# Kernel optimization log

Measured on AMD Instinct MI355X. Metric: run time of the kernel, lower is better.

## Reference

```python
import jax, jax.numpy as jnp
import numpy as np

DIM, H, DH = 3072, 24, 128
MLP = int(DIM * 4.0)
EPS = 1e-6


def setup_inputs() -> dict:
    key = jax.random.key(0)
    ks = jax.random.split(key, 8)
    B, L = 2, 4096
    s = 0.02
    return {
        "hidden_states": jax.random.normal(ks[0], (B, L, DIM), jnp.float32),
        "temb": jax.random.normal(ks[1], (B, DIM), jnp.float32),
        "rope": jax.random.normal(ks[2], (L, DH // 2, 4), jnp.float32),
        "w_lin": jax.random.normal(ks[3], (DIM, 3 * DIM), jnp.float32) * s,
        "b_lin": jnp.zeros((3 * DIM,), jnp.float32),
        "w1": jax.random.normal(ks[4], (DIM, 3 * DIM + MLP), jnp.float32) * s,
        "b1": jnp.zeros((3 * DIM + MLP,), jnp.float32),
        "w2": jax.random.normal(ks[5], (DIM + MLP, DIM), jnp.float32) * s,
        "b2": jnp.zeros((DIM,), jnp.float32),
        "q_scale": jnp.ones((DH,), jnp.float32),
        "k_scale": jnp.ones((DH,), jnp.float32),
    }


def _rms(x, scale):
    return x * jax.lax.rsqrt(jnp.mean(x * x, axis=-1, keepdims=True) + EPS) * scale


def _rope(x, fr):
    # x: [B,H,L,DH]; fr: [L, DH//2, 2, 2]
    B, Hn, L, D = x.shape
    x_ = x.reshape(B, Hn, L, D // 2, 1, 2)
    out = fr[..., 0] * x_[..., 0] + fr[..., 1] * x_[..., 1]  # [B,H,L,D//2,2]
    return out.reshape(B, Hn, L, D)


def reference(hidden_states, temb, rope, w_lin, b_lin, w1, b1, w2, b2, q_scale, k_scale):
    B, L, _ = hidden_states.shape
    residual = hidden_states
    # AdaLayerNormZeroSingle
    emb = jax.nn.silu(temb) @ w_lin + b_lin  # [B, 3*DIM]
    shift, scale, gate = jnp.split(emb[:, None, :], 3, axis=-1)
    mu = jnp.mean(hidden_states, axis=-1, keepdims=True)
    var = jnp.mean(jnp.square(hidden_states - mu), axis=-1, keepdims=True)
    x = (hidden_states - mu) * jax.lax.rsqrt(var + EPS)
    x = x * (1 + scale) + shift
    # fused QKV + MLP projection
    proj = x @ w1 + b1
    qkv, mlp = proj[..., : 3 * DIM], proj[..., 3 * DIM :]
    qkv = qkv.reshape(B, L, 3, H, DH).transpose(2, 0, 3, 1, 4)  # [3,B,H,L,DH]
    q, k, v = qkv[0], qkv[1], qkv[2]
    q = _rms(q, q_scale)
    k = _rms(k, k_scale)
    fr = rope.reshape(L, DH // 2, 2, 2)
    q = _rope(q, fr)
    k = _rope(k, fr)
    # heads are MERGED before attention (faithful to source)
    q = q.transpose(0, 2, 1, 3).reshape(B, L, H * DH)
    k = k.transpose(0, 2, 1, 3).reshape(B, L, H * DH)
    v = v.transpose(0, 2, 1, 3).reshape(B, L, H * DH)
    attn = jax.nn.softmax(jnp.einsum("bqd,bkd->bqk", q, k) * (DH ** -0.5), axis=-1)
    attn_out = jnp.einsum("bqk,bkd->bqd", attn, v)
    h = jnp.concatenate([attn_out, jax.nn.gelu(mlp)], axis=-1) @ w2 + b2
    return residual + gate * h
```

## Files before the change

### kernel.cpp

```cpp
#include <hip/hip_runtime.h>
#include <hip/hip_fp16.h>

typedef _Float16 half_t;
typedef __attribute__((ext_vector_type(8))) _Float16 f16x8;
typedef __attribute__((ext_vector_type(4))) float f32x4;

#define DIM   3072
#define NH    24
#define DH    128
#define MLP_D 12288
#define LSEQ  4096
#define BATCH 2
#define NROWS 8192
#define N1    21504
#define QKV_N 9216
#define CAT_N 15360

__device__ __forceinline__ void gload16(const void* g, void* l) {
  __builtin_amdgcn_global_load_lds((const __attribute__((address_space(1))) void*)g,
                                   (__attribute__((address_space(3))) void*)l, 16, 0, 0);
}

__device__ __forceinline__ float gelu_tanh(float x) {
  float u = 0.7978845608028654f * (x + 0.044715f * x * x * x);
  float t = 1.f - 2.f / (__expf(2.f * u) + 1.f);
  return 0.5f * x * (1.f + t);
}

struct EpiParams {
  const float* bias;
  float* outF; int ldoF;
  half_t* o1; int ldo1;
  half_t* o2; int ldo2;
  const float* resid;
  const float* gate;
  float scale;
};

template<int EPI>
__global__ __launch_bounds__(512, 2) void gemm256(
    const half_t* __restrict__ A, int lda,
    const half_t* __restrict__ B, int ldb,
    int nbx, int nby, int nsplit, int K, EpiParams ep)
{
  __shared__ __align__(16) char lds[131072];
  const int t = threadIdx.x, lane = t & 63, wid = t >> 6;

  const int nwg = nbx * nby;
  const int wg = blockIdx.x;
  const int id = (wg & 7) * (nwg >> 3) + (wg >> 3);
  const int panel = 8 * nbx;
  const int bm = (id / panel) * 8 + (id % 8);
  const int bn = (id % panel) / 8;
  const int brow = bm * 256, bcol = bn * 256;
  const int wr = wid >> 2, wc = wid & 3;

  f32x4 acc[8][4];
#pragma unroll
  for (int m = 0; m < 8; ++m)
#pragma unroll
    for (int n = 0; n < 4; ++n) acc[m][n] = (f32x4){0.f, 0.f, 0.f, 0.f};

  const int scol = (((lane & 3) ^ ((lane >> 3) & 3)) * 8);
  const half_t* pA = A + (size_t)(brow + wid * 32 + (lane >> 2)) * lda + scol;
  const half_t* pB = B + (size_t)(bcol + wid * 32 + (lane >> 2)) * ldb + scol;
  const int wrow = wid * 2048;
  const int NT = K >> 6;

  const int pc = (((lane >> 4) ^ ((lane >> 1) & 3)) << 4);
  const int aoff = (wr * 128 + (lane & 15)) * 64 + pc;
  const int boff = 32768 + (wc * 64 + (lane & 15)) * 64 + pc;

  f16x8 af[2][4], bf[2][4];

#define STAGE_A(bb, kh, tk) {                                               \
    gload16(pA + (size_t)(tk) * 64 + (kh) * 32,                             \
            (bb) + (kh) * 16384 + wrow);                                    \
    gload16(pA + (size_t)(tk) * 64 + (kh) * 32 + (size_t)16 * lda,          \
            (bb) + (kh) * 16384 + wrow + 1024); }
#define STAGE_B(bb, kh, tk) {                                               \
    gload16(pB + (size_t)(tk) * 64 + (kh) * 32,                             \
            (bb) + 32768 + (kh) * 16384 + wrow);                            \
    gload16(pB + (size_t)(tk) * 64 + (kh) * 32 + (size_t)16 * ldb,          \
            (bb) + 32768 + (kh) * 16384 + wrow + 1024); }

#define MFMA_Q(accoff, ab, bb2)                                             \
    _Pragma("unroll")                                                       \
    for (int mi = 0; mi < 4; ++mi)                                          \
      _Pragma("unroll")                                                     \
      for (int nj = 0; nj < 4; ++nj)                                        \
        acc[(accoff) + mi][nj] = __builtin_amdgcn_mfma_f32_16x16x32_f16(    \
            af[ab][mi], bf[bb2][nj], acc[(accoff) + mi][nj], 0, 0, 0);

  {
    char* b0 = lds;
    char* b1 = lds + 65536;
    STAGE_B(b0, 0, 0); STAGE_A(b0, 0, 0); STAGE_B(b0, 1, 0); STAGE_A(b0, 1, 0);
    STAGE_B(b1, 0, 1); STAGE_A(b1, 0, 1); STAGE_B(b1, 1, 1); STAGE_A(b1, 1, 1);
    asm volatile("s_waitcnt vmcnt(8)" ::: "memory");
    __builtin_amdgcn_s_barrier();
#pragma unroll
    for (int mi = 0; mi < 4; ++mi) af[0][mi] = *(const f16x8*)(lds + aoff + mi * 1024);
#pragma unroll
    for (int nj = 0; nj < 4; ++nj) bf[0][nj] = *(const f16x8*)(lds + boff + nj * 1024);
    __builtin_amdgcn_s_barrier();
  }

  for (int tt = 0; tt < NT; ++tt) {
    char* cb = lds + (size_t)(tt & 1) * 65536;
    char* nb = lds + (size_t)((tt & 1) ^ 1) * 65536;

    __builtin_amdgcn_s_setprio(1);
    MFMA_Q(0, 0, 0)
    __builtin_amdgcn_s_setprio(0);
#pragma unroll
    for (int mi = 0; mi < 4; ++mi) af[1][mi] = *(const f16x8*)(cb + aoff + 4096 + mi * 1024);
    if (tt + 2 < NT) STAGE_B(cb, 0, tt + 2);
    __builtin_amdgcn_s_barrier();

    __builtin_amdgcn_s_setprio(1);
    MFMA_Q(4, 1, 0)
    __builtin_amdgcn_s_setprio(0);
#pragma unroll
    for (int mi = 0; mi < 4; ++mi) af[0][mi] = *(const f16x8*)(cb + aoff + 16384 + mi * 1024);
#pragma unroll
    for (int nj = 0; nj < 4; ++nj) bf[1][nj] = *(const f16x8*)(cb + boff + 16384 + nj * 1024);
    if (tt + 2 < NT) STAGE_A(cb, 0, tt + 2);
    __builtin_amdgcn_s_barrier();

    __builtin_amdgcn_s_setprio(1);
    MFMA_Q(0, 0, 1)
    __builtin_amdgcn_s_setprio(0);
#pragma unroll
    for (int mi = 0; mi < 4; ++mi) af[1][mi] = *(const f16x8*)(cb + aoff + 16384 + 4096 + mi * 1024);
    if (tt + 2 < NT) STAGE_B(cb, 1, tt + 2);
    if (tt + 2 < NT) asm volatile("s_waitcnt vmcnt(6)" ::: "memory");
    else             asm volatile("s_waitcnt vmcnt(0)" ::: "memory");
    __builtin_amdgcn_s_barrier();

    __builtin_amdgcn_s_setprio(1);
    MFMA_Q(4, 1, 1)
    __builtin_amdgcn_s_setprio(0);
    if (tt + 1 < NT) {
#pragma unroll
      for (int mi = 0; mi < 4; ++mi) af[0][mi] = *(const f16x8*)(nb + aoff + mi * 1024);
#pragma unroll
      for (int nj = 0; nj < 4; ++nj) bf[0][nj] = *(const f16x8*)(nb + boff + nj * 1024);
    }
    if (tt + 2 < NT) STAGE_A(cb, 1, tt + 2);
    __builtin_amdgcn_s_barrier();
  }
#undef STAGE_A
#undef STAGE_B
#undef MFMA_Q

  const int laneR = lane & 15;
  const int colb = bcol + wc * 64;
  const int rowb = brow + wr * 128 + (lane >> 4) * 4;
#pragma unroll
  for (int mi = 0; mi < 8; ++mi) {
#pragma unroll
    for (int nj = 0; nj < 4; ++nj) {
      int col = colb + nj * 16 + laneR;
#pragma unroll
      for (int j = 0; j < 4; ++j) {
        int row = rowb + mi * 16 + j;
        float v = acc[mi][nj][j];
        if (EPI == 0) {
          v += ep.bias[col];
          if (col < nsplit) {
            ep.o1[(size_t)row * ep.ldo1 + col] = (half_t)v;
          } else {
            ep.o2[(size_t)row * ep.ldo2 + DIM + (col - nsplit)] = (half_t)gelu_tanh(v);
          }
        } else if (EPI == 1) {
          ep.o1[(size_t)row * ep.ldo1 + col] = (half_t)(v * ep.scale);
        } else if (EPI == 2) {
          ep.o2[(size_t)row * ep.ldo2 + col] = (half_t)v;
        } else {
          v += ep.bias[col];
          int b = row >> 12;
          float g = ep.gate[(size_t)b * QKV_N + col];
          float r = ep.resid[(size_t)row * DIM + col];
          ep.outF[(size_t)row * ep.ldoF + col] = r + g * v;
        }
      }
    }
  }
}

__global__ __launch_bounds__(256) void k_emb(
    const float* __restrict__ temb, const float* __restrict__ w_lin,
    const float* __restrict__ b_lin, float* __restrict__ emb)
{
  __shared__ float s[DIM];
  int b = blockIdx.y;
  int col = blockIdx.x * 256 + threadIdx.x;
  const float* tr = temb + (size_t)b * DIM;
  for (int k = threadIdx.x; k < DIM; k += 256) {
    float x = tr[k];
    s[k] = x / (1.f + __expf(-x));
  }
  __syncthreads();
  float acc = b_lin[col];
  for (int k = 0; k < DIM; k += 4) {
    acc += s[k] * w_lin[(size_t)k * QKV_N + col]
         + s[k + 1] * w_lin[(size_t)(k + 1) * QKV_N + col]
         + s[k + 2] * w_lin[(size_t)(k + 2) * QKV_N + col]
         + s[k + 3] * w_lin[(size_t)(k + 3) * QKV_N + col];
  }
  emb[(size_t)b * QKV_N + col] = acc;
}

__global__ __launch_bounds__(256) void k_lnmod(
    const float* __restrict__ hs, const float* __restrict__ emb,
    half_t* __restrict__ xmod)
{
  int row = blockIdx.x;
  int b = row >> 12;
  const float* x = hs + (size_t)row * DIM;
  int t = threadIdx.x;
  float s = 0.f, s2 = 0.f;
  float4 v[3];
#pragma unroll
  for (int i = 0; i < 3; ++i) {
    v[i] = ((const float4*)x)[t + 256 * i];
    s  += v[i].x + v[i].y + v[i].z + v[i].w;
    s2 += v[i].x * v[i].x + v[i].y * v[i].y + v[i].z * v[i].z + v[i].w * v[i].w;
  }
  for (int o = 32; o; o >>= 1) { s += __shfl_xor(s, o); s2 += __shfl_xor(s2, o); }
  __shared__ float rs[4], rs2[4];
  int lane = t & 63, w = t >> 6;
  if (lane == 0) { rs[w] = s; rs2[w] = s2; }
  __syncthreads();
  s = rs[0] + rs[1] + rs[2] + rs[3];
  s2 = rs2[0] + rs2[1] + rs2[2] + rs2[3];
  float mu = s * (1.f / DIM);
  float var = s2 * (1.f / DIM) - mu * mu;
  float rstd = rsqrtf(var + 1e-6f);
  const float* shift = emb + (size_t)b * QKV_N;
  const float* scale = shift + DIM;
#pragma unroll
  for (int i = 0; i < 3; ++i) {
    int g = t + 256 * i;
    float4 sc = ((const float4*)scale)[g];
    float4 sh = ((const float4*)shift)[g];
    half_t ob[4];
    float vv[4] = {v[i].x, v[i].y, v[i].z, v[i].w};
    float scv[4] = {sc.x, sc.y, sc.z, sc.w};
    float shv[4] = {sh.x, sh.y, sh.z, sh.w};
#pragma unroll
    for (int j = 0; j < 4; ++j) {
      float xn = (vv[j] - mu) * rstd;
      ob[j] = (half_t)(xn * (1.f + scv[j]) + shv[j]);
    }
    *(uint2*)&xmod[(size_t)row * DIM + g * 4] = *(uint2*)ob;
  }
}

__global__ __launch_bounds__(256) void k_transpose_cvt(
    const float* __restrict__ in, half_t* __restrict__ out, int R, int C)
{
  __shared__ float s[64][65];
  int c0 = blockIdx.x * 64, r0 = blockIdx.y * 64;
  int tx = threadIdx.x & 63, ty = threadIdx.x >> 6;
#pragma unroll
  for (int j = 0; j < 16; ++j) {
    int r = ty + j * 4;
    s[r][tx] = in[(size_t)(r0 + r) * C + c0 + tx];
  }
  __syncthreads();
#pragma unroll
  for (int j = 0; j < 16; ++j) {
    int c = ty + j * 4;
    out[(size_t)(c0 + c) * R + r0 + tx] = (half_t)s[tx][c];
  }
}

__global__ __launch_bounds__(256) void k_qk_rmsrope(
    half_t* __restrict__ qkv, const float* __restrict__ rope,
    const float* __restrict__ q_scale, const float* __restrict__ k_scale)
{
  int w = blockIdx.x * 4 + (threadIdx.x >> 6);
  int lane = threadIdx.x & 63;
  int qk = w & 1;
  int hr = w >> 1;
  int h = hr % 24;
  int bl = hr / 24;
  size_t base = (size_t)bl * QKV_N + qk * DIM + h * DH;
  float x0 = (float)qkv[base + lane * 2];
  float x1 = (float)qkv[base + lane * 2 + 1];
  float ss = x0 * x0 + x1 * x1;
  for (int o = 32; o; o >>= 1) ss += __shfl_xor(ss, o);
  float r = rsqrtf(ss * (1.f / DH) + 1e-6f);
  const float* sc = qk ? k_scale : q_scale;
  float xs0 = x0 * r * sc[lane * 2];
  float xs1 = x1 * r * sc[lane * 2 + 1];
  int l = bl & (LSEQ - 1);
  float4 fr = ((const float4*)rope)[(size_t)l * 64 + lane];
  qkv[base + lane * 2]     = (half_t)(fr.x * xs0 + fr.y * xs1);
  qkv[base + lane * 2 + 1] = (half_t)(fr.z * xs0 + fr.w * xs1);
}

__global__ __launch_bounds__(256) void k_vT(
    const half_t* __restrict__ qkv, half_t* __restrict__ vT)
{
  __shared__ half_t s[64][65];
  int b = blockIdx.z;
  int l0 = blockIdx.x * 64, d0 = blockIdx.y * 64;
  int tx = threadIdx.x & 63, ty = threadIdx.x >> 6;
#pragma unroll
  for (int j = 0; j < 16; ++j) {
    int l = ty + j * 4;
    s[l][tx] = qkv[(size_t)(b * LSEQ + l0 + l) * QKV_N + 2 * DIM + d0 + tx];
  }
  __syncthreads();
#pragma unroll
  for (int j = 0; j < 16; ++j) {
    int d = ty + j * 4;
    vT[((size_t)b * DIM + d0 + d) * LSEQ + l0 + tx] = s[tx][d];
  }
}

__global__ __launch_bounds__(256) void k_softmax(
    const half_t* __restrict__ S, half_t* __restrict__ P)
{
  int row = blockIdx.x;
  const half_t* srow = S + (size_t)row * LSEQ;
  int t = threadIdx.x;
  f16x8 hv[2];
  float vf[16];
  float mx = -1e30f;
#pragma unroll
  for (int i = 0; i < 2; ++i) {
    hv[i] = ((const f16x8*)srow)[t + 256 * i];
#pragma unroll
    for (int j = 0; j < 8; ++j) {
      vf[i * 8 + j] = (float)hv[i][j];
      mx = fmaxf(mx, vf[i * 8 + j]);
    }
  }
  for (int o = 32; o; o >>= 1) mx = fmaxf(mx, __shfl_xor(mx, o));
  __shared__ float rmx[4], rsum[4];
  int lane = t & 63, w = t >> 6;
  if (lane == 0) rmx[w] = mx;
  __syncthreads();
  mx = fmaxf(fmaxf(rmx[0], rmx[1]), fmaxf(rmx[2], rmx[3]));
  float s = 0.f;
#pragma unroll
  for (int i = 0; i < 16; ++i) {
    vf[i] = __expf(vf[i] - mx);
    s += vf[i];
  }
  for (int o = 32; o; o >>= 1) s += __shfl_xor(s, o);
  if (lane == 0) rsum[w] = s;
  __syncthreads();
  s = rsum[0] + rsum[1] + rsum[2] + rsum[3];
  float inv = 1.f / s;
#pragma unroll
  for (int i = 0; i < 2; ++i) {
    f16x8 ob;
#pragma unroll
    for (int j = 0; j < 8; ++j) ob[j] = (half_t)(vf[i * 8 + j] * inv);
    ((f16x8*)&P[(size_t)row * LSEQ])[t + 256 * i] = ob;
  }
}

extern "C" void kernel_launch(void* const* d_in, const int* in_sizes, int n_in,
                              void* d_out, int out_size, void* d_ws, size_t ws_size,
                              hipStream_t stream) {
  const float* hs      = (const float*)d_in[0];
  const float* temb    = (const float*)d_in[1];
  const float* rope    = (const float*)d_in[2];
  const float* w_lin   = (const float*)d_in[3];
  const float* b_lin   = (const float*)d_in[4];
  const float* w1      = (const float*)d_in[5];
  const float* b1      = (const float*)d_in[6];
  const float* w2      = (const float*)d_in[7];
  const float* b2      = (const float*)d_in[8];
  const float* q_scale = (const float*)d_in[9];
  const float* k_scale = (const float*)d_in[10];
  float* out = (float*)d_out;

  char* ws = (char*)d_ws;
  size_t off = 0;
  auto alloc = [&](size_t bytes) { char* p = ws + off; off += (bytes + 255) & ~(size_t)255; return p; };
  float*  emb    = (float*) alloc((size_t)BATCH * QKV_N * 4);
  half_t* xmod   = (half_t*)alloc((size_t)NROWS * DIM * 2);
  half_t* w1T    = (half_t*)alloc((size_t)N1 * DIM * 2);
  half_t* w2T    = (half_t*)alloc((size_t)DIM * CAT_N * 2);
  half_t* qkv    = (half_t*)alloc((size_t)NROWS * QKV_N * 2);
  half_t* concat = (half_t*)alloc((size_t)NROWS * CAT_N * 2);
  half_t* vT     = (half_t*)alloc((size_t)BATCH * DIM * LSEQ * 2);
  half_t* Sbuf   = (half_t*)alloc((size_t)LSEQ * LSEQ * 2);
  half_t* Pbuf   = (half_t*)alloc((size_t)LSEQ * LSEQ * 2);
  (void)ws_size; (void)n_in; (void)in_sizes; (void)out_size;

  k_emb<<<dim3(QKV_N / 256, BATCH), 256, 0, stream>>>(temb, w_lin, b_lin, emb);
  k_transpose_cvt<<<dim3(N1 / 64, DIM / 64), 256, 0, stream>>>(w1, w1T, DIM, N1);
  k_transpose_cvt<<<dim3(DIM / 64, CAT_N / 64), 256, 0, stream>>>(w2, w2T, CAT_N, DIM);
  k_lnmod<<<NROWS, 256, 0, stream>>>(hs, emb, xmod);

  EpiParams ep1 = {b1, nullptr, 0, qkv, QKV_N, concat, CAT_N, nullptr, nullptr, 0.f};
  gemm256<0><<<(N1 / 256) * (NROWS / 256), 512, 0, stream>>>(
      xmod, DIM, w1T, DIM, N1 / 256, NROWS / 256, QKV_N, DIM, ep1);

  k_qk_rmsrope<<<(NROWS * NH * 2) / 4, 256, 0, stream>>>(qkv, rope, q_scale, k_scale);
  k_vT<<<dim3(LSEQ / 64, DIM / 64, BATCH), 256, 0, stream>>>(qkv, vT);

  for (int b = 0; b < BATCH; ++b) {
    const half_t* qb = qkv + (size_t)b * LSEQ * QKV_N;
    EpiParams epS = {nullptr, nullptr, 0, Sbuf, LSEQ, nullptr, 0, nullptr, nullptr, 0.08838834764831845f};
    gemm256<1><<<(LSEQ / 256) * (LSEQ / 256), 512, 0, stream>>>(
        qb, QKV_N, qb + DIM, QKV_N, LSEQ / 256, LSEQ / 256, 0, DIM, epS);
    k_softmax<<<LSEQ, 256, 0, stream>>>(Sbuf, Pbuf);
    EpiParams epPV = {nullptr, nullptr, 0, nullptr, 0,
                      concat + (size_t)b * LSEQ * CAT_N, CAT_N, nullptr, nullptr, 0.f};
    gemm256<2><<<(DIM / 256) * (LSEQ / 256), 512, 0, stream>>>(
        Pbuf, LSEQ, vT + (size_t)b * DIM * LSEQ, LSEQ, DIM / 256, LSEQ / 256, 0, LSEQ, epPV);
  }

  EpiParams ep2 = {b2, out, DIM, nullptr, 0, nullptr, 0, hs, emb + 2 * DIM, 0.f};
  gemm256<3><<<(DIM / 256) * (NROWS / 256), 512, 0, stream>>>(
      concat, CAT_N, w2T, CAT_N, DIM / 256, NROWS / 256, 0, CAT_N, ep2);
}
```

Baseline: 2.788 ms.

## Batch attention GEMMs across batch and merge small prologue kernels

Result: no change. 2.779 ms (-0.3%).

```diff
diff --git a/kernel.cpp b/kernel.cpp
--- a/kernel.cpp
+++ b/kernel.cpp
@@ -41,19 +41,24 @@
 __global__ __launch_bounds__(512, 2) void gemm256(
     const half_t* __restrict__ A, int lda,
     const half_t* __restrict__ B, int ldb,
-    int nbx, int nby, int nsplit, int K, EpiParams ep)
+    int nbx, int nper, size_t strA, size_t strB, size_t strO,
+    int nsplit, int K, EpiParams ep)
 {
   __shared__ __align__(16) char lds[131072];
   const int t = threadIdx.x, lane = t & 63, wid = t >> 6;
 
-  const int nwg = nbx * nby;
+  const int nwg = gridDim.x;
   const int wg = blockIdx.x;
   const int id = (wg & 7) * (nwg >> 3) + (wg >> 3);
+  const int bz = id / nper;
+  const int rid = id - bz * nper;
   const int panel = 8 * nbx;
-  const int bm = (id / panel) * 8 + (id % 8);
-  const int bn = (id % panel) / 8;
+  const int bm = (rid / panel) * 8 + (rid % 8);
+  const int bn = (rid % panel) / 8;
   const int brow = bm * 256, bcol = bn * 256;
   const int wr = wid >> 2, wc = wid & 3;
+  A += bz * strA;
+  B += bz * strB;
 
   f32x4 acc[8][4];
 #pragma unroll
@@ -154,6 +159,10 @@
 #undef STAGE_B
 #undef MFMA_Q
 
+  half_t* o1 = ep.o1;
+  half_t* o2 = ep.o2;
+  if (EPI == 1) o1 += (size_t)bz * strO;
+  if (EPI == 2) o2 += (size_t)bz * strO;
   const int laneR = lane & 15;
   const int colb = bcol + wc * 64;
   const int rowb = brow + wr * 128 + (lane >> 4) * 4;
@@ -169,14 +178,14 @@
         if (EPI == 0) {
           v += ep.bias[col];
           if (col < nsplit) {
-            ep.o1[(size_t)row * ep.ldo1 + col] = (half_t)v;
+            o1[(size_t)row * ep.ldo1 + col] = (half_t)v;
           } else {
-            ep.o2[(size_t)row * ep.ldo2 + DIM + (col - nsplit)] = (half_t)gelu_tanh(v);
+            o2[(size_t)row * ep.ldo2 + DIM + (col - nsplit)] = (half_t)gelu_tanh(v);
           }
         } else if (EPI == 1) {
-          ep.o1[(size_t)row * ep.ldo1 + col] = (half_t)(v * ep.scale);
+          o1[(size_t)row * ep.ldo1 + col] = (half_t)(v * ep.scale);
         } else if (EPI == 2) {
-          ep.o2[(size_t)row * ep.ldo2 + col] = (half_t)v;
+          o2[(size_t)row * ep.ldo2 + col] = (half_t)v;
         } else {
           v += ep.bias[col];
           int b = row >> 12;
@@ -189,27 +198,71 @@
   }
 }
 
-__global__ __launch_bounds__(256) void k_emb(
+__device__ __forceinline__ void tp_tile(
+    const float* __restrict__ in, half_t* __restrict__ out, int R, int C,
+    int r0, int c0, float (*s)[65], int t)
+{
+  const int tx = t & 15, ty = t >> 4;
+#pragma unroll
+  for (int j = 0; j < 4; ++j) {
+    int r = ty + j * 16;
+    float4 v = *(const float4*)&in[(size_t)(r0 + r) * C + c0 + tx * 4];
+    s[r][tx * 4 + 0] = v.x; s[r][tx * 4 + 1] = v.y;
+    s[r][tx * 4 + 2] = v.z; s[r][tx * 4 + 3] = v.w;
+  }
+  __syncthreads();
+#pragma unroll
+  for (int j = 0; j < 4; ++j) {
+    int c = ty + j * 16;
+    half_t o[4] = {(half_t)s[tx * 4 + 0][c], (half_t)s[tx * 4 + 1][c],
+                   (half_t)s[tx * 4 + 2][c], (half_t)s[tx * 4 + 3][c]};
+    *(uint2*)&out[(size_t)(c0 + c) * R + r0 + tx * 4] = *(uint2*)o;
+  }
+}
+
+#define NBW1 ((N1 / 64) * (DIM / 64))
+#define NBW2 ((DIM / 64) * (CAT_N / 64))
+#define NBEMB ((QKV_N / 256) * BATCH)
+
+__global__ __launch_bounds__(256) void k_pre(
+    const float* __restrict__ w1, half_t* __restrict__ w1T,
+    const float* __restrict__ w2, half_t* __restrict__ w2T,
     const float* __restrict__ temb, const float* __restrict__ w_lin,
     const float* __restrict__ b_lin, float* __restrict__ emb)
 {
-  __shared__ float s[DIM];
-  int b = blockIdx.y;
-  int col = blockIdx.x * 256 + threadIdx.x;
-  const float* tr = temb + (size_t)b * DIM;
-  for (int k = threadIdx.x; k < DIM; k += 256) {
-    float x = tr[k];
-    s[k] = x / (1.f + __expf(-x));
-  }
-  __syncthreads();
-  float acc = b_lin[col];
-  for (int k = 0; k < DIM; k += 4) {
-    acc += s[k] * w_lin[(size_t)k * QKV_N + col]
-         + s[k + 1] * w_lin[(size_t)(k + 1) * QKV_N + col]
-         + s[k + 2] * w_lin[(size_t)(k + 2) * QKV_N + col]
-         + s[k + 3] * w_lin[(size_t)(k + 3) * QKV_N + col];
-  }
-  emb[(size_t)b * QKV_N + col] = acc;
+  __shared__ float s[64][65];
+  int id = blockIdx.x;
+  if (id < NBW1) {
+    int cx = id % (N1 / 64), ry = id / (N1 / 64);
+    tp_tile(w1, w1T, DIM, N1, ry * 64, cx * 64, s, threadIdx.x);
+    return;
+  }
+  id -= NBW1;
+  if (id < NBW2) {
+    int cx = id % (DIM / 64), ry = id / (DIM / 64);
+    tp_tile(w2, w2T, CAT_N, DIM, ry * 64, cx * 64, s, threadIdx.x);
+    return;
+  }
+  id -= NBW2;
+  {
+    float* sf = &s[0][0];
+    int b = id / (QKV_N / 256);
+    int col = (id % (QKV_N / 256)) * 256 + threadIdx.x;
+    const float* tr = temb + (size_t)b * DIM;
+    for (int k = threadIdx.x; k < DIM; k += 256) {
+      float x = tr[k];
+      sf[k] = x / (1.f + __expf(-x));
+    }
+    __syncthreads();
+    float acc = b_lin[col];
+    for (int k = 0; k < DIM; k += 4) {
+      acc += sf[k] * w_lin[(size_t)k * QKV_N + col]
+           + sf[k + 1] * w_lin[(size_t)(k + 1) * QKV_N + col]
+           + sf[k + 2] * w_lin[(size_t)(k + 2) * QKV_N + col]
+           + sf[k + 3] * w_lin[(size_t)(k + 3) * QKV_N + col];
+    }
+    emb[(size_t)b * QKV_N + col] = acc;
+  }
 }
 
 __global__ __launch_bounds__(256) void k_lnmod(
@@ -258,67 +311,56 @@
   }
 }
 
-__global__ __launch_bounds__(256) void k_transpose_cvt(
-    const float* __restrict__ in, half_t* __restrict__ out, int R, int C)
-{
-  __shared__ float s[64][65];
-  int c0 = blockIdx.x * 64, r0 = blockIdx.y * 64;
-  int tx = threadIdx.x & 63, ty = threadIdx.x >> 6;
-#pragma unroll
-  for (int j = 0; j < 16; ++j) {
-    int r = ty + j * 4;
-    s[r][tx] = in[(size_t)(r0 + r) * C + c0 + tx];
-  }
-  __syncthreads();
-#pragma unroll
-  for (int j = 0; j < 16; ++j) {
-    int c = ty + j * 4;
-    out[(size_t)(c0 + c) * R + r0 + tx] = (half_t)s[tx][c];
-  }
-}
-
-__global__ __launch_bounds__(256) void k_qk_rmsrope(
+#define NROPE ((NROWS * NH * 2) / 4)
+#define NVT   ((LSEQ / 64) * (DIM / 64) * BATCH)
+
+__global__ __launch_bounds__(256) void k_ropevt(
     half_t* __restrict__ qkv, const float* __restrict__ rope,
-    const float* __restrict__ q_scale, const float* __restrict__ k_scale)
-{
-  int w = blockIdx.x * 4 + (threadIdx.x >> 6);
-  int lane = threadIdx.x & 63;
-  int qk = w & 1;
-  int hr = w >> 1;
-  int h = hr % 24;
-  int bl = hr / 24;
-  size_t base = (size_t)bl * QKV_N + qk * DIM + h * DH;
-  float x0 = (float)qkv[base + lane * 2];
-  float x1 = (float)qkv[base + lane * 2 + 1];
-  float ss = x0 * x0 + x1 * x1;
-  for (int o = 32; o; o >>= 1) ss += __shfl_xor(ss, o);
-  float r = rsqrtf(ss * (1.f / DH) + 1e-6f);
-  const float* sc = qk ? k_scale : q_scale;
-  float xs0 = x0 * r * sc[lane * 2];
-  float xs1 = x1 * r * sc[lane * 2 + 1];
-  int l = bl & (LSEQ - 1);
-  float4 fr = ((const float4*)rope)[(size_t)l * 64 + lane];
-  qkv[base + lane * 2]     = (half_t)(fr.x * xs0 + fr.y * xs1);
-  qkv[base + lane * 2 + 1] = (half_t)(fr.z * xs0 + fr.w * xs1);
-}
-
-__global__ __launch_bounds__(256) void k_vT(
-    const half_t* __restrict__ qkv, half_t* __restrict__ vT)
+    const float* __restrict__ q_scale, const float* __restrict__ k_scale,
+    half_t* __restrict__ vT)
 {
   __shared__ half_t s[64][65];
-  int b = blockIdx.z;
-  int l0 = blockIdx.x * 64, d0 = blockIdx.y * 64;
-  int tx = threadIdx.x & 63, ty = threadIdx.x >> 6;
-#pragma unroll
-  for (int j = 0; j < 16; ++j) {
-    int l = ty + j * 4;
-    s[l][tx] = qkv[(size_t)(b * LSEQ + l0 + l) * QKV_N + 2 * DIM + d0 + tx];
-  }
-  __syncthreads();
-#pragma unroll
-  for (int j = 0; j < 16; ++j) {
-    int d = ty + j * 4;
-    vT[((size_t)b * DIM + d0 + d) * LSEQ + l0 + tx] = s[tx][d];
+  int id = blockIdx.x;
+  if (id < NROPE) {
+    int w = id * 4 + (threadIdx.x >> 6);
+    int lane = threadIdx.x & 63;
+    int qk = w & 1;
+    int hr = w >> 1;
+    int h = hr % 24;
+    int bl = hr / 24;
+    size_t base = (size_t)bl * QKV_N + qk * DIM + h * DH;
+    float x0 = (float)qkv[base + lane * 2];
+    float x1 = (float)qkv[base + lane * 2 + 1];
+    float ss = x0 * x0 + x1 * x1;
+    for (int o = 32; o; o >>= 1) ss += __shfl_xor(ss, o);
+    float r = rsqrtf(ss * (1.f / DH) + 1e-6f);
+    const float* sc = qk ? k_scale : q_scale;
+    float xs0 = x0 * r * sc[lane * 2];
+    float xs1 = x1 * r * sc[lane * 2 + 1];
+    int l = bl & (LSEQ - 1);
+    float4 fr = ((const float4*)rope)[(size_t)l * 64 + lane];
+    qkv[base + lane * 2]     = (half_t)(fr.x * xs0 + fr.y * xs1);
+    qkv[base + lane * 2 + 1] = (half_t)(fr.z * xs0 + fr.w * xs1);
+    return;
+  }
+  id -= NROPE;
+  {
+    int nb = (LSEQ / 64) * (DIM / 64);
+    int b = id / nb;
+    int rem = id % nb;
+    int l0 = (rem % (LSEQ / 64)) * 64, d0 = (rem / (LSEQ / 64)) * 64;
+    int tx = threadIdx.x & 63, ty = threadIdx.x >> 6;
+#pragma unroll
+    for (int j = 0; j < 16; ++j) {
+      int l = ty + j * 4;
+      s[l][tx] = qkv[(size_t)(b * LSEQ + l0 + l) * QKV_N + 2 * DIM + d0 + tx];
+    }
+    __syncthreads();
+#pragma unroll
+    for (int j = 0; j < 16; ++j) {
+      int d = ty + j * 4;
+      vT[((size_t)b * DIM + d0 + d) * LSEQ + l0 + tx] = s[tx][d];
+    }
   }
 }
 
@@ -392,35 +434,34 @@
   half_t* qkv    = (half_t*)alloc((size_t)NROWS * QKV_N * 2);
   half_t* concat = (half_t*)alloc((size_t)NROWS * CAT_N * 2);
   half_t* vT     = (half_t*)alloc((size_t)BATCH * DIM * LSEQ * 2);
-  half_t* Sbuf   = (half_t*)alloc((size_t)LSEQ * LSEQ * 2);
-  half_t* Pbuf   = (half_t*)alloc((size_t)LSEQ * LSEQ * 2);
+  half_t* Sbuf   = (half_t*)alloc((size_t)BATCH * LSEQ * LSEQ * 2);
+  half_t* Pbuf   = (half_t*)alloc((size_t)BATCH * LSEQ * LSEQ * 2);
   (void)ws_size; (void)n_in; (void)in_sizes; (void)out_size;
 
-  k_emb<<<dim3(QKV_N / 256, BATCH), 256, 0, stream>>>(temb, w_lin, b_lin, emb);
-  k_transpose_cvt<<<dim3(N1 / 64, DIM / 64), 256, 0, stream>>>(w1, w1T, DIM, N1);
-  k_transpose_cvt<<<dim3(DIM / 64, CAT_N / 64), 256, 0, stream>>>(w2, w2T, CAT_N, DIM);
+  k_pre<<<NBW1 + NBW2 + NBEMB, 256, 0, stream>>>(w1, w1T, w2, w2T, temb, w_lin, b_lin, emb);
   k_lnmod<<<NROWS, 256, 0, stream>>>(hs, emb, xmod);
 
   EpiParams ep1 = {b1, nullptr, 0, qkv, QKV_N, concat, CAT_N, nullptr, nullptr, 0.f};
   gemm256<0><<<(N1 / 256) * (NROWS / 256), 512, 0, stream>>>(
-      xmod, DIM, w1T, DIM, N1 / 256, NROWS / 256, QKV_N, DIM, ep1);
-
-  k_qk_rmsrope<<<(NROWS * NH * 2) / 4, 256, 0, stream>>>(qkv, rope, q_scale, k_scale);
-  k_vT<<<dim3(LSEQ / 64, DIM / 64, BATCH), 256, 0, stream>>>(qkv, vT);
-
-  for (int b = 0; b < BATCH; ++b) {
-    const half_t* qb = qkv + (size_t)b * LSEQ * QKV_N;
-    EpiParams epS = {nullptr, nullptr, 0, Sbuf, LSEQ, nullptr, 0, nullptr, nullptr, 0.08838834764831845f};
-    gemm256<1><<<(LSEQ / 256) * (LSEQ / 256), 512, 0, stream>>>(
-        qb, QKV_N, qb + DIM, QKV_N, LSEQ / 256, LSEQ / 256, 0, DIM, epS);
-    k_softmax<<<LSEQ, 256, 0, stream>>>(Sbuf, Pbuf);
-    EpiParams epPV = {nullptr, nullptr, 0, nullptr, 0,
-                      concat + (size_t)b * LSEQ * CAT_N, CAT_N, nullptr, nullptr, 0.f};
-    gemm256<2><<<(DIM / 256) * (LSEQ / 256), 512, 0, stream>>>(
-        Pbuf, LSEQ, vT + (size_t)b * DIM * LSEQ, LSEQ, DIM / 256, LSEQ / 256, 0, LSEQ, epPV);
-  }
+      xmod, DIM, w1T, DIM, N1 / 256, (N1 / 256) * (NROWS / 256), 0, 0, 0, QKV_N, DIM, ep1);
+
+  k_ropevt<<<NROPE + NVT, 256, 0, stream>>>(qkv, rope, q_scale, k_scale, vT);
+
+  EpiParams epS = {nullptr, nullptr, 0, Sbuf, LSEQ, nullptr, 0, nullptr, nullptr, 0.08838834764831845f};
+  gemm256<1><<<(LSEQ / 256) * (LSEQ / 256) * BATCH, 512, 0, stream>>>(
+      qkv, QKV_N, qkv + DIM, QKV_N,
+      LSEQ / 256, (LSEQ / 256) * (LSEQ / 256),
+      (size_t)LSEQ * QKV_N, (size_t)LSEQ * QKV_N, (size_t)LSEQ * LSEQ,
+      0, DIM, epS);
+  k_softmax<<<BATCH * LSEQ, 256, 0, stream>>>(Sbuf, Pbuf);
+  EpiParams epPV = {nullptr, nullptr, 0, nullptr, 0, concat, CAT_N, nullptr, nullptr, 0.f};
+  gemm256<2><<<(DIM / 256) * (LSEQ / 256) * BATCH, 512, 0, stream>>>(
+      Pbuf, LSEQ, vT, LSEQ,
+      DIM / 256, (DIM / 256) * (LSEQ / 256),
+      (size_t)LSEQ * LSEQ, (size_t)DIM * LSEQ, (size_t)LSEQ * CAT_N,
+      0, LSEQ, epPV);
 
   EpiParams ep2 = {b2, out, DIM, nullptr, 0, nullptr, 0, hs, emb + 2 * DIM, 0.f};
   gemm256<3><<<(DIM / 256) * (NROWS / 256), 512, 0, stream>>>(
-      concat, CAT_N, w2T, CAT_N, DIM / 256, NROWS / 256, 0, CAT_N, ep2);
-}
+      concat, CAT_N, w2T, CAT_N, DIM / 256, (DIM / 256) * (NROWS / 256), 0, 0, 0, 0, CAT_N, ep2);
+}
```
